# Kernel tuning notes

Measured on AMD Instinct MI355X. Metric: run time of the kernel, lower is better.

The kernel has to match this reference:

```python
import jax, jax.numpy as jnp
import numpy as np

B, C, HID, H, W_ = 16, 2048, 256, 32, 32

def setup_inputs() -> dict:
    key = jax.random.key(0)
    k1, k2, k3 = jax.random.split(key, 3)
    return {
        "query_features": jax.random.normal(k1, (B, C, H, W_), dtype=jnp.float32),
        "prompt_features": jax.random.normal(k2, (B, C, H, W_), dtype=jnp.float32),
        "W": jax.random.normal(k3, (HID, C), dtype=jnp.float32) * 0.02,
        "b": jnp.zeros((HID,), dtype=jnp.float32),
    }

def reference(query_features, prompt_features, W, b):
    Bq, Cc, Hh, Ww = query_features.shape
    HW = Hh * Ww
    # 1x1 conv == channel matmul
    Q = jnp.einsum('oc,bchw->bohw', W, query_features) + b[None, :, None, None]
    K = jnp.einsum('oc,bchw->bohw', W, prompt_features) + b[None, :, None, None]
    Qf = Q.reshape(Bq, -1, HW)          # (b, hid, HW1)
    Kf = K.reshape(Bq, -1, HW)          # (b, hid, HW2)
    Vf = prompt_features.reshape(Bq, Cc, HW)  # (b, C, HW2)
    scores = jnp.einsum('bcq,bck->bqk', Qf, Kf)   # (b, HW1, HW2)
    A = jax.nn.softmax(scores, axis=-1)
    aligned = jnp.einsum('bqk,bck->bcq', A, Vf).reshape(Bq, Cc, Hh, Ww)
    # fusion_policy == 'cat'
    return jnp.concatenate([query_features, aligned], axis=1)
```

## Files before the change

kernel.cpp:

```cpp
#include <hip/hip_runtime.h>

#define NB   16
#define NC   2048
#define NHID 256
#define NHW  1024

using half2_t  = __attribute__((ext_vector_type(2))) _Float16;
using half4_t  = __attribute__((ext_vector_type(4))) _Float16;
using half8_t  = __attribute__((ext_vector_type(8))) _Float16;
using float4_t = __attribute__((ext_vector_type(4))) float;

#define OUT_BATCH_BYTES ((size_t)(4096u * 1024u) * 4u)

__device__ __forceinline__ void async_load16(const void* g, void* l) {
    __builtin_amdgcn_global_load_lds((__attribute__((address_space(1))) void*)g,
                                     (__attribute__((address_space(3))) void*)l, 16, 0, 0);
}

template <int NROWS>
__device__ __forceinline__ void stage_async(const _Float16* __restrict__ src, size_t stride_h,
                                            _Float16* __restrict__ lds, int t) {
    #pragma unroll
    for (int i = 0; i < NROWS / 32; ++i) {
        const int o   = i * 4096 + t * 16;
        const int row = o >> 7;
        const int s   = ((o >> 4) & 7) ^ (row & 7);
        const _Float16* g = src + (size_t)row * stride_h + s * 8;
        async_load16(g, (char*)lds + o);
    }
}

__device__ __forceinline__ void stage_async512(const _Float16* __restrict__ src, size_t stride_h,
                                               _Float16* __restrict__ lds, int t) {
    #pragma unroll
    for (int i = 0; i < 4; ++i) {
        const int o   = i * 8192 + t * 16;
        const int row = o >> 7;
        const int s   = ((o >> 4) & 7) ^ (row & 7);
        const _Float16* g = src + (size_t)row * stride_h + s * 8;
        async_load16(g, (char*)lds + o);
    }
}

__device__ __forceinline__ half8_t frag_read(const _Float16* __restrict__ lds, int row, int kk, int quad) {
    const int s = (kk * 4 + quad) ^ (row & 7);
    return *(const half8_t*)((const char*)lds + row * 128 + s * 16);
}

#define ACC_INIT(acc) \
    _Pragma("unroll") for (int i_ = 0; i_ < 4; ++i_) \
    _Pragma("unroll") for (int j_ = 0; j_ < 4; ++j_) \
    _Pragma("unroll") for (int r_ = 0; r_ < 4; ++r_) acc[i_][j_][r_] = 0.f;

__device__ __forceinline__ void gemm_f16(const _Float16* __restrict__ A, size_t lda,
                                         const _Float16* __restrict__ B, size_t ldb,
                                         int K, _Float16* __restrict__ As, _Float16* __restrict__ Bs,
                                         float4_t acc[4][4]) {
    const int t = threadIdx.x;
    const int l = t & 63, quad = l >> 4, l15 = l & 15;
    const int w = t >> 6;
    const int wr = (w >> 1) * 64, wc = (w & 1) * 64;
    for (int k0 = 0; k0 < K; k0 += 64) {
        stage_async<128>(A + k0, lda, As, t);
        stage_async<128>(B + k0, ldb, Bs, t);
        __syncthreads();
        #pragma unroll
        for (int kk = 0; kk < 2; ++kk) {
            half8_t af[4], bf[4];
            #pragma unroll
            for (int i = 0; i < 4; ++i) af[i] = frag_read(As, wr + i * 16 + l15, kk, quad);
            #pragma unroll
            for (int j = 0; j < 4; ++j) bf[j] = frag_read(Bs, wc + j * 16 + l15, kk, quad);
            #pragma unroll
            for (int i = 0; i < 4; ++i)
                #pragma unroll
                for (int j = 0; j < 4; ++j)
                    acc[i][j] = __builtin_amdgcn_mfma_f32_16x16x32_f16(af[i], bf[j], acc[i][j], 0, 0, 0);
        }
        __syncthreads();
    }
}

__global__ __launch_bounds__(256) void wcvt_kernel(const float* __restrict__ W, _Float16* __restrict__ W16) {
    const int idx = (blockIdx.x * 256 + threadIdx.x) * 8;
    float4 a = *(const float4*)(W + idx);
    float4 c = *(const float4*)(W + idx + 4);
    half8_t h;
    h[0] = (_Float16)a.x; h[1] = (_Float16)a.y; h[2] = (_Float16)a.z; h[3] = (_Float16)a.w;
    h[4] = (_Float16)c.x; h[5] = (_Float16)c.y; h[6] = (_Float16)c.z; h[7] = (_Float16)c.w;
    *(half8_t*)(W16 + idx) = h;
}

__global__ __launch_bounds__(512, 4) void proj16_kernel(
    const float* __restrict__ qf, const float* __restrict__ pf,
    const _Float16* __restrict__ W16, const float* __restrict__ bias,
    _Float16* __restrict__ Q16, _Float16* __restrict__ K16,
    float* __restrict__ out) {
    __shared__ __attribute__((aligned(16))) _Float16 As[64 * 72];
    __shared__ __attribute__((aligned(16))) _Float16 Bs[256 * 64];
    const int z = blockIdx.z, which = z >> 4, b = z & 15;
    const float* X = (which ? pf : qf) + (size_t)b * NC * NHW;
    float*     passq = (float*)((char*)out + (size_t)b * OUT_BATCH_BYTES);
    _Float16*  V16   = (_Float16*)((char*)out + (size_t)b * OUT_BATCH_BYTES);
    _Float16* O = (which ? K16 : Q16) + (size_t)b * NHW * NHID;
    const int m0 = blockIdx.x * 64;
    const int t = threadIdx.x;
    const int l = t & 63, quad = l >> 4, l15 = l & 15;
    const int w = t >> 6;
    const int wr = (w >> 2) * 32;
    const int wc = (w & 3) * 64;
    const int j  = t & 15;
    const int gs = t >> 4;

    float4_t acc[2][4];
    #pragma unroll
    for (int i = 0; i < 2; ++i)
        #pragma unroll
        for (int jj = 0; jj < 4; ++jj)
            #pragma unroll
            for (int r = 0; r < 4; ++r) acc[i][jj][r] = 0.f;

    for (int k0 = 0; k0 < NC; k0 += 64) {
        const int c0 = k0 + gs * 2;
        float4 x0 = *(const float4*)(X + (size_t)c0 * NHW + m0 + j * 4);
        float4 x1 = *(const float4*)(X + (size_t)(c0 + 1) * NHW + m0 + j * 4);
        half4_t hv0, hv1;
        #pragma unroll
        for (int e = 0; e < 4; ++e) { hv0[e] = (_Float16)((&x0.x)[e]); hv1[e] = (_Float16)((&x1.x)[e]); }
        if (which) {
            *(half4_t*)(V16 + (size_t)c0 * NHW + m0 + j * 4)       = hv0;
            *(half4_t*)(V16 + (size_t)(c0 + 1) * NHW + m0 + j * 4) = hv1;
        } else if (k0 >= 1024) {
            *(float4*)(passq + (size_t)c0 * NHW + m0 + j * 4)       = x0;
            *(float4*)(passq + (size_t)(c0 + 1) * NHW + m0 + j * 4) = x1;
        }
        #pragma unroll
        for (int e = 0; e < 4; ++e) {
            half2_t h2; h2[0] = hv0[e]; h2[1] = hv1[e];
            *(half2_t*)(As + (j * 4 + e) * 72 + gs * 2) = h2;
        }
        stage_async512(W16 + k0, NC, Bs, t);
        __syncthreads();
        #pragma unroll
        for (int kk = 0; kk < 2; ++kk) {
            half8_t af[2], bf[4];
            #pragma unroll
            for (int i = 0; i < 2; ++i)
                af[i] = *(const half8_t*)(As + (wr + i * 16 + l15) * 72 + kk * 32 + quad * 8);
            #pragma unroll
            for (int jj = 0; jj < 4; ++jj)
                bf[jj] = frag_read(Bs, wc + jj * 16 + l15, kk, quad);
            #pragma unroll
            for (int i = 0; i < 2; ++i)
                #pragma unroll
                for (int jj = 0; jj < 4; ++jj)
                    acc[i][jj] = __builtin_amdgcn_mfma_f32_16x16x32_f16(af[i], bf[jj], acc[i][jj], 0, 0, 0);
        }
        __syncthreads();
    }
    #pragma unroll
    for (int jj = 0; jj < 4; ++jj) {
        const float bv = bias[wc + jj * 16 + l15];
        #pragma unroll
        for (int i = 0; i < 2; ++i)
            #pragma unroll
            for (int r = 0; r < 4; ++r) {
                int hw  = m0 + wr + i * 16 + quad * 4 + r;
                int hid = wc + jj * 16 + l15;
                O[(size_t)hw * NHID + hid] = (_Float16)(acc[i][jj][r] + bv);
            }
    }
}

__global__ __launch_bounds__(256) void scores16_kernel(
    const _Float16* __restrict__ Q16, const _Float16* __restrict__ K16, float* __restrict__ S) {
    __shared__ __attribute__((aligned(16))) _Float16 As[8192];
    __shared__ __attribute__((aligned(16))) _Float16 Bs[8192];
    const int oid = blockIdx.x + blockIdx.y * 8 + blockIdx.z * 64;
    const int xcd = oid & 7, half = (oid >> 9) & 1, r = (oid >> 3) & 63;
    const int b = xcd * 2 + half;
    const int m0 = (r >> 3) * 128, n0 = (r & 7) * 128;
    float* Sb = S + (size_t)b * NHW * NHW;
    float4_t acc[4][4];
    ACC_INIT(acc)
    gemm_f16(Q16 + (size_t)b * NHW * NHID + (size_t)m0 * NHID, NHID,
             K16 + (size_t)b * NHW * NHID + (size_t)n0 * NHID, NHID, NHID, As, Bs, acc);
    const int t = threadIdx.x, l = t & 63, quad = l >> 4, l15 = l & 15, w = t >> 6;
    const int wr = (w >> 1) * 64, wc = (w & 1) * 64;
    #pragma unroll
    for (int i = 0; i < 4; ++i)
        #pragma unroll
        for (int j = 0; j < 4; ++j)
            #pragma unroll
            for (int rr = 0; rr < 4; ++rr) {
                int q1 = m0 + wr + i * 16 + quad * 4 + rr;
                int q2 = n0 + wc + j * 16 + l15;
                Sb[(size_t)q1 * NHW + q2] = acc[i][j][rr];
            }
}

__global__ __launch_bounds__(256) void softmax_kernel(float* __restrict__ S) {
    const int t = threadIdx.x, wave = t >> 6, lane = t & 63;
    float* row = S + ((size_t)blockIdx.x * 4 + wave) * NHW;
    float4 v[4];
    float mx = -1e30f;
    #pragma unroll
    for (int j = 0; j < 4; ++j) {
        v[j] = *(const float4*)(row + (lane << 2) + (j << 8));
        mx = fmaxf(mx, fmaxf(fmaxf(v[j].x, v[j].y), fmaxf(v[j].z, v[j].w)));
    }
    #pragma unroll
    for (int off = 32; off >= 1; off >>= 1) mx = fmaxf(mx, __shfl_xor(mx, off, 64));
    float s = 0.f;
    #pragma unroll
    for (int j = 0; j < 4; ++j) {
        v[j].x = __expf(v[j].x - mx); v[j].y = __expf(v[j].y - mx);
        v[j].z = __expf(v[j].z - mx); v[j].w = __expf(v[j].w - mx);
        s += v[j].x + v[j].y + v[j].z + v[j].w;
    }
    #pragma unroll
    for (int off = 32; off >= 1; off >>= 1) s += __shfl_xor(s, off, 64);
    const float inv = 1.0f / s;
    __syncthreads();
    _Float16* o = (_Float16*)row;
    #pragma unroll
    for (int j = 0; j < 4; ++j) {
        half4_t h;
        h[0] = (_Float16)(v[j].x * inv); h[1] = (_Float16)(v[j].y * inv);
        h[2] = (_Float16)(v[j].z * inv); h[3] = (_Float16)(v[j].w * inv);
        *(half4_t*)(o + (lane << 2) + (j << 8)) = h;
    }
}

__global__ __launch_bounds__(256) void av16_kernel(
    const float* __restrict__ S, float* __restrict__ out) {
    __shared__ __attribute__((aligned(16))) _Float16 As[8192];
    __shared__ __attribute__((aligned(16))) _Float16 Bs[8192];
    const int oid = blockIdx.x + blockIdx.y * 8 + blockIdx.z * 128;
    const int xcd = oid & 7, half = (oid >> 10) & 1, r = (oid >> 3) & 127;
    const int b = xcd * 2 + half;
    const int m0 = (r >> 3) * 128;
    const int n0 = (r & 7) * 128;
    const _Float16* Vb  = (const _Float16*)((const char*)out + (size_t)b * OUT_BATCH_BYTES);
    const _Float16* A16 = (const _Float16*)(S + (size_t)b * NHW * NHW);
    float* Ob = out + (size_t)b * (2 * NC) * NHW + (size_t)NC * NHW;
    float4_t acc[4][4];
    ACC_INIT(acc)
    gemm_f16(Vb + (size_t)m0 * NHW, NHW, A16 + (size_t)n0 * 2048, 2048, NHW, As, Bs, acc);
    const int t = threadIdx.x, l = t & 63, quad = l >> 4, l15 = l & 15, w = t >> 6;
    const int wr = (w >> 1) * 64, wc = (w & 1) * 64;
    #pragma unroll
    for (int i = 0; i < 4; ++i)
        #pragma unroll
        for (int j = 0; j < 4; ++j)
            #pragma unroll
            for (int rr = 0; rr < 4; ++rr) {
                int c = m0 + wr + i * 16 + quad * 4 + rr;
                int q = n0 + wc + j * 16 + l15;
                Ob[(size_t)c * NHW + q] = acc[i][j][rr];
            }
}

__global__ __launch_bounds__(256) void copy2_kernel(const uint4* __restrict__ qf,
                                                    uint4* __restrict__ out) {
    const int idx = blockIdx.x * 256 + threadIdx.x;
    const int b = idx >> 18;
    const int r = idx & 0x3FFFF;
    out[((size_t)b << 20) + r] = qf[((size_t)b << 19) + r];
}

extern "C" void kernel_launch(void* const* d_in, const int* in_sizes, int n_in,
                              void* d_out, int out_size, void* d_ws, size_t ws_size,
                              hipStream_t stream) {
    const float* qf   = (const float*)d_in[0];
    const float* pf   = (const float*)d_in[1];
    const float* Wm   = (const float*)d_in[2];
    const float* bias = (const float*)d_in[3];
    float* out = (float*)d_out;

    float*    S   = (float*)d_ws;
    _Float16* Q16 = (_Float16*)((char*)d_ws + ((size_t)64 << 20));
    _Float16* K16 = (_Float16*)((char*)d_ws + ((size_t)72 << 20));
    _Float16* W16 = (_Float16*)((char*)out + ((size_t)8 << 20));

    wcvt_kernel<<<256, 256, 0, stream>>>(Wm, W16);
    proj16_kernel<<<dim3(16, 1, 32), 512, 0, stream>>>(qf, pf, W16, bias, Q16, K16, out);
    scores16_kernel<<<dim3(8, 8, 16), 256, 0, stream>>>(Q16, K16, S);
    softmax_kernel<<<NB * 256, 256, 0, stream>>>(S);
    av16_kernel<<<dim3(8, 16, 16), 256, 0, stream>>>(S, out);
    copy2_kernel<<<16384, 256, 0, stream>>>((const uint4*)qf, (uint4*)out);
}
```

Before: 612.5 us.

## Drop fp16 V staging and copy kernel; convert prompt features inside AV GEMM

The projection kernel no longer writes an fp16 copy of prompt features into the output buffer, and now writes the whole query passthrough itself, so the separate copy kernel is removed. The AV kernel reads fp32 prompt features directly, converts them to fp16 in registers and writes a swizzled LDS tile, with register prefetch of the next tile. The projection loop also prefetches the next input tile into registers. This removes a scratch write and a full copy pass, but the AV GEMM now reads fp32 V tiles repeatedly across column blocks.

After: 590.9 us. 3.5% less time.

```diff
diff --git a/kernel.cpp b/kernel.cpp
--- a/kernel.cpp
+++ b/kernel.cpp
@@ -100,8 +100,7 @@
     __shared__ __attribute__((aligned(16))) _Float16 Bs[256 * 64];
     const int z = blockIdx.z, which = z >> 4, b = z & 15;
     const float* X = (which ? pf : qf) + (size_t)b * NC * NHW;
-    float*     passq = (float*)((char*)out + (size_t)b * OUT_BATCH_BYTES);
-    _Float16*  V16   = (_Float16*)((char*)out + (size_t)b * OUT_BATCH_BYTES);
+    float* passq = (float*)((char*)out + (size_t)b * OUT_BATCH_BYTES);
     _Float16* O = (which ? K16 : Q16) + (size_t)b * NHW * NHID;
     const int m0 = blockIdx.x * 64;
     const int t = threadIdx.x;
@@ -120,26 +119,29 @@
             #pragma unroll
             for (int r = 0; r < 4; ++r) acc[i][jj][r] = 0.f;
 
+    const float* X0 = X + (size_t)(gs * 2) * NHW + m0 + j * 4;
+    float4 x0 = *(const float4*)X0;
+    float4 x1 = *(const float4*)(X0 + NHW);
+
     for (int k0 = 0; k0 < NC; k0 += 64) {
-        const int c0 = k0 + gs * 2;
-        float4 x0 = *(const float4*)(X + (size_t)c0 * NHW + m0 + j * 4);
-        float4 x1 = *(const float4*)(X + (size_t)(c0 + 1) * NHW + m0 + j * 4);
-        half4_t hv0, hv1;
-        #pragma unroll
-        for (int e = 0; e < 4; ++e) { hv0[e] = (_Float16)((&x0.x)[e]); hv1[e] = (_Float16)((&x1.x)[e]); }
-        if (which) {
-            *(half4_t*)(V16 + (size_t)c0 * NHW + m0 + j * 4)       = hv0;
-            *(half4_t*)(V16 + (size_t)(c0 + 1) * NHW + m0 + j * 4) = hv1;
-        } else if (k0 >= 1024) {
-            *(float4*)(passq + (size_t)c0 * NHW + m0 + j * 4)       = x0;
-            *(float4*)(passq + (size_t)(c0 + 1) * NHW + m0 + j * 4) = x1;
+        stage_async512(W16 + k0, NC, Bs, t);
+        if (which == 0) {
+            float* pq = passq + (size_t)(k0 + gs * 2) * NHW + m0 + j * 4;
+            *(float4*)pq = x0;
+            *(float4*)(pq + NHW) = x1;
         }
         #pragma unroll
         for (int e = 0; e < 4; ++e) {
-            half2_t h2; h2[0] = hv0[e]; h2[1] = hv1[e];
+            half2_t h2;
+            h2[0] = (_Float16)((&x0.x)[e]);
+            h2[1] = (_Float16)((&x1.x)[e]);
             *(half2_t*)(As + (j * 4 + e) * 72 + gs * 2) = h2;
         }
-        stage_async512(W16 + k0, NC, Bs, t);
+        if (k0 + 64 < NC) {
+            const float* Xn = X + (size_t)(k0 + 64 + gs * 2) * NHW + m0 + j * 4;
+            x0 = *(const float4*)Xn;
+            x1 = *(const float4*)(Xn + NHW);
+        }
         __syncthreads();
         #pragma unroll
         for (int kk = 0; kk < 2; ++kk) {
@@ -233,7 +235,7 @@
 }
 
 __global__ __launch_bounds__(256) void av16_kernel(
-    const float* __restrict__ S, float* __restrict__ out) {
+    const float* __restrict__ pf, const float* __restrict__ S, float* __restrict__ out) {
     __shared__ __attribute__((aligned(16))) _Float16 As[8192];
     __shared__ __attribute__((aligned(16))) _Float16 Bs[8192];
     const int oid = blockIdx.x + blockIdx.y * 8 + blockIdx.z * 128;
@@ -241,14 +243,62 @@
     const int b = xcd * 2 + half;
     const int m0 = (r >> 3) * 128;
     const int n0 = (r & 7) * 128;
-    const _Float16* Vb  = (const _Float16*)((const char*)out + (size_t)b * OUT_BATCH_BYTES);
+    const float* Vb = pf + (size_t)b * NC * NHW;
     const _Float16* A16 = (const _Float16*)(S + (size_t)b * NHW * NHW);
     float* Ob = out + (size_t)b * (2 * NC) * NHW + (size_t)NC * NHW;
+    const int t = threadIdx.x, l = t & 63, quad = l >> 4, l15 = l & 15, w = t >> 6;
+    const int wr = (w >> 1) * 64, wc = (w & 1) * 64;
+
     float4_t acc[4][4];
     ACC_INIT(acc)
-    gemm_f16(Vb + (size_t)m0 * NHW, NHW, A16 + (size_t)n0 * 2048, 2048, NHW, As, Bs, acc);
-    const int t = threadIdx.x, l = t & 63, quad = l >> 4, l15 = l & 15, w = t >> 6;
-    const int wr = (w >> 1) * 64, wc = (w & 1) * 64;
+
+    float4 vr0[4], vr1[4];
+    #pragma unroll
+    for (int i = 0; i < 4; ++i) {
+        const int flat = i * 256 + t, rr = flat >> 3, ss = flat & 7;
+        const float* p = Vb + (size_t)(m0 + rr) * NHW + ss * 8;
+        vr0[i] = *(const float4*)p;
+        vr1[i] = *(const float4*)(p + 4);
+    }
+
+    for (int k0 = 0; k0 < NHW; k0 += 64) {
+        stage_async<128>(A16 + (size_t)n0 * 2048 + k0, 2048, Bs, t);
+        #pragma unroll
+        for (int i = 0; i < 4; ++i) {
+            const int flat = i * 256 + t, rr = flat >> 3, ss = flat & 7;
+            half8_t h;
+            #pragma unroll
+            for (int e = 0; e < 4; ++e) {
+                h[e]     = (_Float16)((&vr0[i].x)[e]);
+                h[4 + e] = (_Float16)((&vr1[i].x)[e]);
+            }
+            *(half8_t*)((char*)As + rr * 128 + ((ss ^ (rr & 7)) * 16)) = h;
+        }
+        if (k0 + 64 < NHW) {
+            #pragma unroll
+            for (int i = 0; i < 4; ++i) {
+                const int flat = i * 256 + t, rr = flat >> 3, ss = flat & 7;
+                const float* p = Vb + (size_t)(m0 + rr) * NHW + (k0 + 64) + ss * 8;
+                vr0[i] = *(const float4*)p;
+                vr1[i] = *(const float4*)(p + 4);
+            }
+        }
+        __syncthreads();
+        #pragma unroll
+        for (int kk = 0; kk < 2; ++kk) {
+            half8_t af[4], bf[4];
+            #pragma unroll
+            for (int i = 0; i < 4; ++i) af[i] = frag_read(As, wr + i * 16 + l15, kk, quad);
+            #pragma unroll
+            for (int j = 0; j < 4; ++j) bf[j] = frag_read(Bs, wc + j * 16 + l15, kk, quad);
+            #pragma unroll
+            for (int i = 0; i < 4; ++i)
+                #pragma unroll
+                for (int j = 0; j < 4; ++j)
+                    acc[i][j] = __builtin_amdgcn_mfma_f32_16x16x32_f16(af[i], bf[j], acc[i][j], 0, 0, 0);
+        }
+        __syncthreads();
+    }
     #pragma unroll
     for (int i = 0; i < 4; ++i)
         #pragma unroll
@@ -259,14 +309,6 @@
                 int q = n0 + wc + j * 16 + l15;
                 Ob[(size_t)c * NHW + q] = acc[i][j][rr];
             }
-}
-
-__global__ __launch_bounds__(256) void copy2_kernel(const uint4* __restrict__ qf,
-                                                    uint4* __restrict__ out) {
-    const int idx = blockIdx.x * 256 + threadIdx.x;
-    const int b = idx >> 18;
-    const int r = idx & 0x3FFFF;
-    out[((size_t)b << 20) + r] = qf[((size_t)b << 19) + r];
 }
 
 extern "C" void kernel_launch(void* const* d_in, const int* in_sizes, int n_in,
@@ -287,6 +329,5 @@
     proj16_kernel<<<dim3(16, 1, 32), 512, 0, stream>>>(qf, pf, W16, bias, Q16, K16, out);
     scores16_kernel<<<dim3(8, 8, 16), 256, 0, stream>>>(Q16, K16, S);
     softmax_kernel<<<NB * 256, 256, 0, stream>>>(S);
-    av16_kernel<<<dim3(8, 16, 16), 256, 0, stream>>>(S, out);
-    copy2_kernel<<<16384, 256, 0, stream>>>((const uint4*)qf, (uint4*)out);
-}
+    av16_kernel<<<dim3(8, 16, 16), 256, 0, stream>>>(pf, S, out);
+}
```
